# Optimization experiments

Hardware: AMD Instinct MI355X
Metric: run time of the kernel (lower is better)

The kernel has to match this reference:

```python
import jax, jax.numpy as jnp
import numpy as np

B, S, H = 2, 2048, 1024
NH, HD = 16, 64
SCALE = HD ** -0.5


def setup_inputs() -> dict:
    key = jax.random.key(0)
    k1, k2, k3, k4 = jax.random.split(key, 4)
    hidden_states = jax.random.normal(k1, (B, S, H), dtype=jnp.float32)
    attention_mask = jax.random.randint(k2, (B, S), 0, 2, dtype=jnp.int32)
    # xavier-uniform-ish init scale
    w_qkv = jax.random.normal(k3, (3 * H, H), dtype=jnp.float32) * (2.0 / (H + 3 * H)) ** 0.5
    w_out = jax.random.normal(k4, (H, H), dtype=jnp.float32) * (1.0 / H) ** 0.5
    return {"hidden_states": hidden_states, "attention_mask": attention_mask,
            "w_qkv": w_qkv, "w_out": w_out}


def reference(hidden_states, attention_mask, w_qkv, w_out):
    b, s, _ = hidden_states.shape
    qkv = hidden_states @ w_qkv.T                      # [B,S,3H]
    q, k, v = jnp.split(qkv, 3, axis=-1)
    # [B,S,H] -> [B,NH,S,HD]
    reshape = lambda x: x.reshape(b, s, NH, HD).transpose(0, 2, 1, 3)
    q, k, v = reshape(q), reshape(k), reshape(v)
    scores = jnp.einsum('bhqd,bhkd->bhqk', q, k) * SCALE   # [B,NH,S,S]
    mask = attention_mask[:, None, None, :] == 0           # [B,1,1,S]
    scores = jnp.where(mask, -jnp.inf, scores)
    attn = jax.nn.softmax(scores, axis=-1)                 # dropout p: eval mode -> identity
    out = jnp.einsum('bhqk,bhkd->bhqd', attn, v)           # [B,NH,S,HD]
    out = out.transpose(0, 2, 1, 3).reshape(b, s, H)
    return out @ w_out.T
```

## Files before the change

kernel.cpp:

```cpp
#include <hip/hip_runtime.h>
#include <string.h>


typedef __bf16    bf16x8 __attribute__((ext_vector_type(8)));
typedef _Float16  f16x4  __attribute__((ext_vector_type(4)));
typedef _Float16  f16x2  __attribute__((ext_vector_type(2)));
typedef float     f32x4  __attribute__((ext_vector_type(4)));

#define NTOK   4096
#define HDIM   1024
#define SEQ    2048
#define NHEAD  16
#define F2SHIFT 4.0f
#define QSCALE  0.18033688f
#define LSTRIDE 68
#define KHALF  1024

__device__ __forceinline__ float bf2f(unsigned short u) {
    union { unsigned int i; float f; } x;
    x.i = ((unsigned int)u) << 16;
    return x.f;
}
__device__ __forceinline__ unsigned short f2bf(float f) {
    union { __bf16 h; unsigned short u; } x;
    x.h = (__bf16)f;
    return x.u;
}
__device__ __forceinline__ unsigned short f2h(float f) {
    union { _Float16 h; unsigned short u; } x;
    x.h = (_Float16)f;
    return x.u;
}
__device__ __forceinline__ float h2f(unsigned short u) {
    union { unsigned short u; _Float16 h; } x;
    x.u = u;
    return (float)x.h;
}
__device__ __forceinline__ f16x2 pkrtz(float a, float b) {
    union { __fp16 __attribute__((ext_vector_type(2))) i; f16x2 o; } x;
    x.i = __builtin_amdgcn_cvt_pkrtz(a, b);
    return x.o;
}

__device__ __forceinline__ int detect_f32(const unsigned short* hs) {
    unsigned int idx = (threadIdx.x & 63) * 4096u;
    float f = bf2f(hs[idx]);
    return __any(!(fabsf(f) < 1e4f));
}

typedef const __attribute__((address_space(1))) unsigned int* gptr_u32;
typedef __attribute__((address_space(3))) unsigned int* lptr_u32;

__device__ __forceinline__ void async16(const unsigned short* g, unsigned short* l) {
    __builtin_amdgcn_global_load_lds((gptr_u32)g, (lptr_u32)l, 16, 0, 0);
}

__global__ void convert3_kernel(const void* __restrict__ s0, const void* __restrict__ s1,
                                const void* __restrict__ s2, unsigned short* __restrict__ dst) {
    const int isf32 = detect_f32((const unsigned short*)s0);
    if (!isf32) return;
    int g = blockIdx.x * blockDim.x + threadIdx.x;
    const int stride = gridDim.x * blockDim.x;
    for (; g < 1048576; g += stride) {
        int i = g * 8;
        const void* src; int off;
        if (i < 4194304)      { src = s0; off = i; }
        else if (i < 7340032) { src = s1; off = i - 4194304; }
        else                  { src = s2; off = i - 7340032; }
        const float* s = (const float*)src + off;
        unsigned short o[8];
#pragma unroll
        for (int j = 0; j < 8; j++) o[j] = f2bf(s[j]);
        *(uint4*)(dst + i) = *(const uint4*)o;
    }
}

__global__ __launch_bounds__(256) void gemm_qkv(
    const unsigned short* __restrict__ Xc, const unsigned short* __restrict__ Wc,
    const unsigned short* __restrict__ Xraw, const unsigned short* __restrict__ Wraw,
    unsigned short* __restrict__ q_out, unsigned short* __restrict__ k_out,
    unsigned short* __restrict__ v_out) {
    const int K = 1024;
    __shared__ __align__(16) unsigned short Xs0[128 * 32];
    __shared__ __align__(16) unsigned short Xs1[128 * 32];
    __shared__ __align__(16) unsigned short Ws0[128 * 32];
    __shared__ __align__(16) unsigned short Ws1[128 * 32];

    const int isf32 = detect_f32(Xraw);
    const unsigned short* X = isf32 ? Xc : Xraw;
    const unsigned short* W = isf32 ? Wc : Wraw;

    const int t = threadIdx.x;
    const int w = t >> 6, lane = t & 63, quad = lane >> 4, lr = lane & 15;
    const int wrow = (w >> 1) * 64, wcol = (w & 1) * 64;

    const int hid = blockIdx.x;
    const int xcd = hid & 7, r = hid >> 3;
    const int by = xcd * 4 + r / 24;
    const int bx = r % 24;
    const int m0 = by * 128, n0 = bx * 128;
    const bool vblk = (n0 >= 2048);

    f32x4 acc[4][4];
#pragma unroll
    for (int mi = 0; mi < 4; mi++)
#pragma unroll
        for (int ni = 0; ni < 4; ni++) acc[mi][ni] = (f32x4){0.f, 0.f, 0.f, 0.f};

    const int srow = w * 32 + (lane >> 2);
    const int scol = (lane & 3) * 8;
    const unsigned short* xg = X + (size_t)(m0 + srow) * K + scol;
    const unsigned short* wg = W + (size_t)(n0 + srow) * K + scol;
    unsigned short* xl0 = &Xs0[w * 1024];
    unsigned short* xl1 = &Xs1[w * 1024];
    unsigned short* wl0 = &Ws0[w * 1024];
    unsigned short* wl1 = &Ws1[w * 1024];

    for (int k0 = 0; k0 < K; k0 += 64) {
        __syncthreads();
        async16(xg + k0, xl0);
        async16(xg + k0 + 16 * K, xl0 + 512);
        async16(xg + k0 + 32, xl1);
        async16(xg + k0 + 32 + 16 * K, xl1 + 512);
        async16(wg + k0, wl0);
        async16(wg + k0 + 16 * K, wl0 + 512);
        async16(wg + k0 + 32, wl1);
        async16(wg + k0 + 32 + 16 * K, wl1 + 512);
        __syncthreads();
#pragma unroll
        for (int h = 0; h < 2; h++) {
            const unsigned short* Xh = h ? Xs1 : Xs0;
            const unsigned short* Wh = h ? Ws1 : Ws0;
            bf16x8 af[4], bfr[4];
#pragma unroll
            for (int mi = 0; mi < 4; mi++)
                af[mi] = *(const bf16x8*)&Xh[(wrow + mi * 16 + lr) * 32 + quad * 8];
#pragma unroll
            for (int ni = 0; ni < 4; ni++)
                bfr[ni] = *(const bf16x8*)&Wh[(wcol + ni * 16 + lr) * 32 + quad * 8];
            if (!vblk) {
#pragma unroll
                for (int mi = 0; mi < 4; mi++)
#pragma unroll
                    for (int ni = 0; ni < 4; ni++)
                        acc[mi][ni] = __builtin_amdgcn_mfma_f32_16x16x32_bf16(af[mi], bfr[ni], acc[mi][ni], 0, 0, 0);
            } else {
#pragma unroll
                for (int mi = 0; mi < 4; mi++)
#pragma unroll
                    for (int ni = 0; ni < 4; ni++)
                        acc[mi][ni] = __builtin_amdgcn_mfma_f32_16x16x32_bf16(bfr[ni], af[mi], acc[mi][ni], 0, 0, 0);
            }
        }
    }

    if (!vblk) {
#pragma unroll
        for (int mi = 0; mi < 4; mi++)
#pragma unroll
            for (int ni = 0; ni < 4; ni++)
#pragma unroll
                for (int rr = 0; rr < 4; rr++) {
                    int mrow = m0 + wrow + mi * 16 + quad * 4 + rr;
                    int j = n0 + wcol + ni * 16 + lr;
                    float val = acc[mi][ni][rr];
                    int which = j >> 10, rem = j & 1023;
                    int nh = rem >> 6, hd = rem & 63;
                    int b = mrow >> 11, s = mrow & 2047;
                    size_t dst = ((size_t)(b * NHEAD + nh) * SEQ + s) * 64 + hd;
                    if (which == 0) q_out[dst] = f2bf(val * QSCALE);
                    else            k_out[dst] = f2bf(val);
                }
    } else {
#pragma unroll
        for (int mi = 0; mi < 4; mi++)
#pragma unroll
            for (int ni = 0; ni < 4; ni++)
#pragma unroll
                for (int rr = 0; rr < 4; rr++) {
                    int n = n0 + wcol + ni * 16 + quad * 4 + rr;
                    int m = m0 + wrow + mi * 16 + lr;
                    float val = acc[mi][ni][rr];
                    int rem = n & 1023;
                    int nh = rem >> 6, hd = rem & 63;
                    int b = m >> 11, s = m & 2047;
                    size_t dst = ((size_t)(b * NHEAD + nh) * 64 + hd) * SEQ + s;
                    v_out[dst] = f2h(val);
                }
    }
}

__global__ __launch_bounds__(256) void gemm_out(
    const unsigned short* __restrict__ X, const unsigned short* __restrict__ Wc,
    const unsigned short* __restrict__ Wraw,
    void* __restrict__ d_out, const unsigned short* __restrict__ hs_raw) {
    const int K = 1024, N = 1024;
    __shared__ __align__(16) unsigned short Xs0[64 * 32];
    __shared__ __align__(16) unsigned short Xs1[64 * 32];
    __shared__ __align__(16) unsigned short Xs2[64 * 32];
    __shared__ __align__(16) unsigned short Xs3[64 * 32];
    __shared__ __align__(16) unsigned short Ws0[128 * 32];
    __shared__ __align__(16) unsigned short Ws1[128 * 32];
    __shared__ __align__(16) unsigned short Ws2[128 * 32];
    __shared__ __align__(16) unsigned short Ws3[128 * 32];

    const int isf32 = detect_f32(hs_raw);
    const unsigned short* W = isf32 ? Wc : Wraw;

    const int t = threadIdx.x;
    const int w = t >> 6, lane = t & 63, quad = lane >> 4, lr = lane & 15;
    const int wrow = (w >> 1) * 32, wcol = (w & 1) * 64;
    const int m0 = blockIdx.y * 64, n0 = blockIdx.x * 128;

    f32x4 acc[2][4];
#pragma unroll
    for (int mi = 0; mi < 2; mi++)
#pragma unroll
        for (int ni = 0; ni < 4; ni++) acc[mi][ni] = (f32x4){0.f, 0.f, 0.f, 0.f};

    const int sxrow = w * 16 + (lane >> 2);
    const int swrow = w * 32 + (lane >> 2);
    const int scol = (lane & 3) * 8;
    const unsigned short* xg = X + (size_t)(m0 + sxrow) * K + scol;
    const unsigned short* wg = W + (size_t)(n0 + swrow) * K + scol;
    unsigned short* xl[4] = { &Xs0[w * 512], &Xs1[w * 512], &Xs2[w * 512], &Xs3[w * 512] };
    unsigned short* wl[4] = { &Ws0[w * 1024], &Ws1[w * 1024], &Ws2[w * 1024], &Ws3[w * 1024] };

    for (int k0 = 0; k0 < K; k0 += 128) {
        __syncthreads();
#pragma unroll
        for (int j = 0; j < 4; j++) {
            async16(xg + k0 + j * 32, xl[j]);
            async16(wg + k0 + j * 32, wl[j]);
            async16(wg + k0 + j * 32 + 16 * K, wl[j] + 512);
        }
        __syncthreads();
#pragma unroll
        for (int h = 0; h < 4; h++) {
            const unsigned short* Xh = (h == 0) ? Xs0 : (h == 1) ? Xs1 : (h == 2) ? Xs2 : Xs3;
            const unsigned short* Wh = (h == 0) ? Ws0 : (h == 1) ? Ws1 : (h == 2) ? Ws2 : Ws3;
            bf16x8 af[2], bfr[4];
#pragma unroll
            for (int mi = 0; mi < 2; mi++)
                af[mi] = *(const bf16x8*)&Xh[(wrow + mi * 16 + lr) * 32 + quad * 8];
#pragma unroll
            for (int ni = 0; ni < 4; ni++)
                bfr[ni] = *(const bf16x8*)&Wh[(wcol + ni * 16 + lr) * 32 + quad * 8];
#pragma unroll
            for (int mi = 0; mi < 2; mi++)
#pragma unroll
                for (int ni = 0; ni < 4; ni++)
                    acc[mi][ni] = __builtin_amdgcn_mfma_f32_16x16x32_bf16(af[mi], bfr[ni], acc[mi][ni], 0, 0, 0);
        }
    }

#pragma unroll
    for (int mi = 0; mi < 2; mi++)
#pragma unroll
        for (int ni = 0; ni < 4; ni++)
#pragma unroll
            for (int rr = 0; rr < 4; rr++) {
                int mrow = m0 + wrow + mi * 16 + quad * 4 + rr;
                int j = n0 + wcol + ni * 16 + lr;
                float val = acc[mi][ni][rr];
                size_t dst = (size_t)mrow * N + j;
                if (isf32) ((float*)d_out)[dst] = val;
                else ((unsigned short*)d_out)[dst] = f2bf(val);
            }
}

__global__ __launch_bounds__(256, 2) void flash_attn_v13(
    const unsigned short* __restrict__ q, const unsigned short* __restrict__ k,
    const unsigned short* __restrict__ vt, const int* __restrict__ mask,
    unsigned short* __restrict__ attn_out,
    unsigned short* __restrict__ opart, float* __restrict__ lpart,
    const int kbase) {
    __shared__ __align__(16) unsigned short Ks[128 * LSTRIDE];
    __shared__ __align__(16) unsigned short Vt0[64 * LSTRIDE];
    __shared__ __align__(16) unsigned short Vt1[64 * LSTRIDE];
    __shared__ __align__(16) float Msk[136];

    const int t = threadIdx.x;
    const int w = t >> 6, lane = t & 63, quad = lane >> 4, lr = lane & 15;
    const int bh = blockIdx.x, b = bh >> 4, h = bh & 15;
    const int q0 = blockIdx.y * 128;

    const unsigned short* qb = q + (size_t)bh * SEQ * 64;
    const unsigned short* kb = k + (size_t)bh * SEQ * 64;
    const unsigned short* vtb = vt + (size_t)bh * 64 * SEQ;
    const int* mb = mask + b * SEQ;

    bf16x8 qf[2][2];
#pragma unroll
    for (int qg = 0; qg < 2; qg++) {
        const unsigned short* qrow = qb + (size_t)(q0 + w * 32 + qg * 16 + lr) * 64 + quad * 8;
        qf[qg][0] = *(const bf16x8*)qrow;
        qf[qg][1] = *(const bf16x8*)(qrow + 32);
    }

    f32x4 oacc[2][4];
#pragma unroll
    for (int qg = 0; qg < 2; qg++)
#pragma unroll
        for (int dt = 0; dt < 4; dt++) oacc[qg][dt] = (f32x4){0.f, 0.f, 0.f, 0.f};
    float l_st[2] = {0.f, 0.f};

    const int sr = t >> 2;
    const int sc = (t & 3) * 16;

    for (int kk0 = kbase; kk0 < kbase + KHALF; kk0 += 128) {
        const uint4* kp0 = (const uint4*)(kb + (size_t)(kk0 + sr) * 64 + sc);
        const uint4* kp1 = (const uint4*)(kb + (size_t)(kk0 + 64 + sr) * 64 + sc);
        const uint4* vp0 = (const uint4*)(vtb + (size_t)sr * SEQ + kk0 + sc);
        const uint4* vp1 = (const uint4*)(vtb + (size_t)sr * SEQ + kk0 + 64 + sc);
        uint4 k0a = kp0[0], k0b = kp0[1];
        uint4 k1a = kp1[0], k1b = kp1[1];
        uint4 v0a = vp0[0], v0b = vp0[1];
        uint4 v1a = vp1[0], v1b = vp1[1];
        float mval = 0.f;
        if (t < 128) mval = (mb[kk0 + t] == 0) ? -1e30f : -F2SHIFT;

        __syncthreads();
        *(uint4*)&Ks[sr * LSTRIDE + sc] = k0a;
        *(uint4*)&Ks[sr * LSTRIDE + sc + 8] = k0b;
        *(uint4*)&Ks[(64 + sr) * LSTRIDE + sc] = k1a;
        *(uint4*)&Ks[(64 + sr) * LSTRIDE + sc + 8] = k1b;
        *(uint4*)&Vt0[sr * LSTRIDE + sc] = v0a;
        *(uint4*)&Vt0[sr * LSTRIDE + sc + 8] = v0b;
        *(uint4*)&Vt1[sr * LSTRIDE + sc] = v1a;
        *(uint4*)&Vt1[sr * LSTRIDE + sc + 8] = v1b;
        if (t < 128) Msk[t] = mval;
        __syncthreads();

        __builtin_amdgcn_s_setprio(1);
#pragma unroll
        for (int mt = 0; mt < 8; mt++) {
            bf16x8 a1h0 = *(bf16x8*)&Ks[(mt * 16 + lr) * LSTRIDE + quad * 8];
            bf16x8 a1h1 = *(bf16x8*)&Ks[(mt * 16 + lr) * LSTRIDE + 32 + quad * 8];
            const unsigned short* vb_ = (mt < 4) ? Vt0 : Vt1;
            const int mcol = (mt & 3) * 16;
            f16x4 a2[4];
#pragma unroll
            for (int dt = 0; dt < 4; dt++)
                a2[dt] = *(const f16x4*)&vb_[(dt * 16 + lr) * LSTRIDE + mcol + quad * 4];
            float4 mv = *(const float4*)&Msk[mt * 16 + quad * 4];
            f32x4 zi = (f32x4){mv.x, mv.y, mv.z, mv.w};

#pragma unroll
            for (int qg = 0; qg < 2; qg++) {
                f32x4 z = __builtin_amdgcn_mfma_f32_16x16x32_bf16(a1h0, qf[qg][0], zi, 0, 0, 0);
                z = __builtin_amdgcn_mfma_f32_16x16x32_bf16(a1h1, qf[qg][1], z, 0, 0, 0);
                float p0 = __builtin_amdgcn_exp2f(z[0]);
                float p1 = __builtin_amdgcn_exp2f(z[1]);
                float p2 = __builtin_amdgcn_exp2f(z[2]);
                float p3 = __builtin_amdgcn_exp2f(z[3]);
                l_st[qg] += (p0 + p1) + (p2 + p3);
                f16x2 ab = pkrtz(p0, p1);
                f16x2 cd = pkrtz(p2, p3);
                f16x4 b2;
                b2[0] = ab[0]; b2[1] = ab[1]; b2[2] = cd[0]; b2[3] = cd[1];
#pragma unroll
                for (int dt = 0; dt < 4; dt++)
                    oacc[qg][dt] = __builtin_amdgcn_mfma_f32_16x16x16f16(a2[dt], b2, oacc[qg][dt], 0, 0, 0);
            }
        }
        __builtin_amdgcn_s_setprio(0);
    }

    float lsum[2];
#pragma unroll
    for (int qg = 0; qg < 2; qg++) {
        float s = l_st[qg];
        s += __shfl_xor(s, 16);
        s += __shfl_xor(s, 32);
        lsum[qg] = s;
    }

    if (kbase == 0) {
#pragma unroll
        for (int qg = 0; qg < 2; qg++) {
            const int qrow = q0 + w * 32 + qg * 16 + lr;
            if (quad == 0) lpart[bh * 2048 + qrow] = lsum[qg];
            size_t tok = (size_t)(b * SEQ + qrow);
#pragma unroll
            for (int dt = 0; dt < 4; dt++)
#pragma unroll
                for (int rr = 0; rr < 4; rr++)
                    opart[tok * HDIM + h * 64 + dt * 16 + quad * 4 + rr] =
                        f2h(oacc[qg][dt][rr]);
        }
    } else {
#pragma unroll
        for (int qg = 0; qg < 2; qg++) {
            const int qrow = q0 + w * 32 + qg * 16 + lr;
            const float inv = 1.0f / (lsum[qg] + lpart[bh * 2048 + qrow]);
            size_t tok = (size_t)(b * SEQ + qrow);
#pragma unroll
            for (int dt = 0; dt < 4; dt++) {
                const unsigned short* op = &opart[tok * HDIM + h * 64 + dt * 16 + quad * 4];
#pragma unroll
                for (int rr = 0; rr < 4; rr++)
                    attn_out[tok * HDIM + h * 64 + dt * 16 + quad * 4 + rr] =
                        f2bf((oacc[qg][dt][rr] + h2f(op[rr])) * inv);
            }
        }
    }
}

extern "C" void kernel_launch(void* const* d_in, const int* in_sizes, int n_in,
                              void* d_out, int out_size, void* d_ws, size_t ws_size,
                              hipStream_t stream) {
    const void* hs_raw = d_in[0];
    const int* mask = (const int*)d_in[1];
    const void* wqkv_raw = d_in[2];
    const void* wout_raw = d_in[3];

    char* wsb = (char*)d_ws;
    unsigned short* hs_c = (unsigned short*)(wsb + 256);
    unsigned short* wqkv_c = hs_c + 4194304;
    unsigned short* wout_c = wqkv_c + 3145728;
    unsigned short* qw = wout_c + 1048576;
    unsigned short* kw = qw + 4194304;
    unsigned short* vtw = kw + 4194304;
    unsigned short* ao = vtw + 4194304;

    unsigned short* opart = hs_c;
    float* lpart = (float*)wqkv_c;

    convert3_kernel<<<1024, 256, 0, stream>>>(hs_raw, wqkv_raw, wout_raw, hs_c);

    gemm_qkv<<<768, 256, 0, stream>>>(hs_c, wqkv_c,
                                      (const unsigned short*)hs_raw,
                                      (const unsigned short*)wqkv_raw,
                                      qw, kw, vtw);
    flash_attn_v13<<<dim3(32, 16), 256, 0, stream>>>(qw, kw, vtw, mask, ao, opart, lpart, 0);
    flash_attn_v13<<<dim3(32, 16), 256, 0, stream>>>(qw, kw, vtw, mask, ao, opart, lpart, 1024);
    gemm_out<<<dim3(8, 64), 256, 0, stream>>>(ao, wout_c,
                                              (const unsigned short*)wout_raw, d_out,
                                              (const unsigned short*)hs_raw);
}
```

Baseline: 195.4 us.

## Pipeline QKV GEMM K-loop with ping-pong LDS halves and MFMA priority

```diff
diff --git a/kernel.cpp b/kernel.cpp
--- a/kernel.cpp
+++ b/kernel.cpp
@@ -116,43 +116,57 @@
     unsigned short* wl0 = &Ws0[w * 1024];
     unsigned short* wl1 = &Ws1[w * 1024];
 
+    async16(xg, xl0);
+    async16(xg + 16 * K, xl0 + 512);
+    async16(wg, wl0);
+    async16(wg + 16 * K, wl0 + 512);
+
+#define QKV_COMPUTE(Xh, Wh)                                                            \
+    {                                                                                  \
+        bf16x8 af[4], bfr[4];                                                          \
+        _Pragma("unroll")                                                              \
+        for (int mi = 0; mi < 4; mi++)                                                 \
+            af[mi] = *(const bf16x8*)&Xh[(wrow + mi * 16 + lr) * 32 + quad * 8];       \
+        _Pragma("unroll")                                                              \
+        for (int ni = 0; ni < 4; ni++)                                                 \
+            bfr[ni] = *(const bf16x8*)&Wh[(wcol + ni * 16 + lr) * 32 + quad * 8];      \
+        __builtin_amdgcn_s_setprio(1);                                                 \
+        if (!vblk) {                                                                   \
+            _Pragma("unroll")                                                          \
+            for (int mi = 0; mi < 4; mi++)                                             \
+                _Pragma("unroll")                                                      \
+                for (int ni = 0; ni < 4; ni++)                                         \
+                    acc[mi][ni] = __builtin_amdgcn_mfma_f32_16x16x32_bf16(             \
+                        af[mi], bfr[ni], acc[mi][ni], 0, 0, 0);                        \
+        } else {                                                                       \
+            _Pragma("unroll")                                                          \
+            for (int mi = 0; mi < 4; mi++)                                             \
+                _Pragma("unroll")                                                      \
+                for (int ni = 0; ni < 4; ni++)                                         \
+                    acc[mi][ni] = __builtin_amdgcn_mfma_f32_16x16x32_bf16(             \
+                        bfr[ni], af[mi], acc[mi][ni], 0, 0, 0);                        \
+        }                                                                              \
+        __builtin_amdgcn_s_setprio(0);                                                 \
+    }
+
     for (int k0 = 0; k0 < K; k0 += 64) {
         __syncthreads();
-        async16(xg + k0, xl0);
-        async16(xg + k0 + 16 * K, xl0 + 512);
         async16(xg + k0 + 32, xl1);
         async16(xg + k0 + 32 + 16 * K, xl1 + 512);
-        async16(wg + k0, wl0);
-        async16(wg + k0 + 16 * K, wl0 + 512);
         async16(wg + k0 + 32, wl1);
         async16(wg + k0 + 32 + 16 * K, wl1 + 512);
-        __syncthreads();
-#pragma unroll
-        for (int h = 0; h < 2; h++) {
-            const unsigned short* Xh = h ? Xs1 : Xs0;
-            const unsigned short* Wh = h ? Ws1 : Ws0;
-            bf16x8 af[4], bfr[4];
-#pragma unroll
-            for (int mi = 0; mi < 4; mi++)
-                af[mi] = *(const bf16x8*)&Xh[(wrow + mi * 16 + lr) * 32 + quad * 8];
-#pragma unroll
-            for (int ni = 0; ni < 4; ni++)
-                bfr[ni] = *(const bf16x8*)&Wh[(wcol + ni * 16 + lr) * 32 + quad * 8];
-            if (!vblk) {
-#pragma unroll
-                for (int mi = 0; mi < 4; mi++)
-#pragma unroll
-                    for (int ni = 0; ni < 4; ni++)
-                        acc[mi][ni] = __builtin_amdgcn_mfma_f32_16x16x32_bf16(af[mi], bfr[ni], acc[mi][ni], 0, 0, 0);
-            } else {
-#pragma unroll
-                for (int mi = 0; mi < 4; mi++)
-#pragma unroll
-                    for (int ni = 0; ni < 4; ni++)
-                        acc[mi][ni] = __builtin_amdgcn_mfma_f32_16x16x32_bf16(bfr[ni], af[mi], acc[mi][ni], 0, 0, 0);
-            }
-        }
-    }
+        QKV_COMPUTE(Xs0, Ws0);
+
+        __syncthreads();
+        if (k0 + 64 < K) {
+            async16(xg + k0 + 64, xl0);
+            async16(xg + k0 + 64 + 16 * K, xl0 + 512);
+            async16(wg + k0 + 64, wl0);
+            async16(wg + k0 + 64 + 16 * K, wl0 + 512);
+        }
+        QKV_COMPUTE(Xs1, Ws1);
+    }
+#undef QKV_COMPUTE
 
     if (!vblk) {
 #pragma unroll
```

Result: no change. 192.0 us (-1.8%).
